# Optimization experiments

Measured on AMD Instinct MI355X. Metric: run time of the kernel, lower is better.

Reference implementation:

```python
import jax, jax.numpy as jnp
import numpy as np

EMBED_DIM = 1024
NUM_HEADS = 16
HEAD_DIM = EMBED_DIM // NUM_HEADS


def setup_inputs() -> dict:
    key = jax.random.key(0)
    ks = jax.random.split(key, 5)
    B, S, D = 2, 2048, EMBED_DIM
    scale = 1.0 / np.sqrt(D)
    x = jax.random.normal(ks[0], (B, S, D), dtype=jnp.float32)
    qkv_w = jax.random.uniform(ks[1], (3 * D, D), dtype=jnp.float32, minval=-scale, maxval=scale)
    qkv_b = jax.random.uniform(ks[2], (3 * D,), dtype=jnp.float32, minval=-scale, maxval=scale)
    out_w = jax.random.uniform(ks[3], (D, D), dtype=jnp.float32, minval=-scale, maxval=scale)
    out_b = jax.random.uniform(ks[4], (D,), dtype=jnp.float32, minval=-scale, maxval=scale)
    return {"x": x, "qkv_w": qkv_w, "qkv_b": qkv_b, "out_w": out_w, "out_b": out_b}


def reference(x, qkv_w, qkv_b, out_w, out_b):
    B, S, D = x.shape
    H, hd = NUM_HEADS, HEAD_DIM
    # QKV projection (torch Linear: y = x @ W^T + b)
    qkv = jnp.einsum('bsd,ed->bse', x, qkv_w) + qkv_b          # [B,S,3D]
    qkv = qkv.reshape(B, S, 3, H, hd)
    q, k, v = (jnp.moveaxis(qkv[:, :, i], 2, 1) for i in range(3))  # each [B,H,S,hd]
    scores = jnp.einsum('bhqd,bhkd->bhqk', q, k) / np.sqrt(hd)  # [B,H,S,S]
    probs = jax.nn.softmax(scores, axis=-1)
    attn = jnp.einsum('bhqk,bhkd->bhqd', probs, v)              # [B,H,S,hd]
    attn = jnp.moveaxis(attn, 1, 2).reshape(B, S, D)
    return jnp.einsum('bsd,ed->bse', attn, out_w) + out_b
```

## Files before the change

### kernel.cpp

```cpp
#include <hip/hip_runtime.h>
#include <stdint.h>

typedef __bf16 bf16;
typedef __attribute__((ext_vector_type(2))) __bf16 bf16x2;
typedef __attribute__((ext_vector_type(4))) __bf16 bf16x4;
typedef __attribute__((ext_vector_type(8))) __bf16 bf16x8;
typedef __attribute__((ext_vector_type(4))) float f32x4;
typedef __attribute__((ext_vector_type(16))) float f32x16;

#define LOG2E_OVER_8 0.18033688011112042f

__device__ __forceinline__ void gl_lds16(const bf16* g, bf16* l) {
  __builtin_amdgcn_global_load_lds(
      (const __attribute__((address_space(1))) void*)g,
      (__attribute__((address_space(3))) void*)l, 16, 0, 0);
}
#define WAIT_VM0_BARRIER() asm volatile("s_waitcnt vmcnt(0)\n\ts_barrier" ::: "memory")

__device__ __forceinline__ uint32_t pack2(float a, float b) {
  union { bf16x2 v; uint32_t u; } z;
  z.v[0] = (bf16)a; z.v[1] = (bf16)b;
  return z.u;
}

__global__ __launch_bounds__(256) void cvt_kernel(const float* __restrict__ s,
                                                  bf16* __restrict__ d, int n) {
  int i = (blockIdx.x * 256 + threadIdx.x) * 8;
  if (i >= n) return;
  float4 a = *(const float4*)(s + i);
  float4 b = *(const float4*)(s + i + 4);
  bf16x8 o;
  o[0] = (bf16)a.x; o[1] = (bf16)a.y; o[2] = (bf16)a.z; o[3] = (bf16)a.w;
  o[4] = (bf16)b.x; o[5] = (bf16)b.y; o[6] = (bf16)b.z; o[7] = (bf16)b.w;
  *(bf16x8*)(d + i) = o;
}

template <int EPI>
__global__ __launch_bounds__(256, 3) void gemm_bt(
    const bf16* __restrict__ A, const bf16* __restrict__ Bw,
    const float* __restrict__ bias,
    bf16* __restrict__ qo, bf16* __restrict__ ko, bf16* __restrict__ vTo,
    float* __restrict__ outF) {
  constexpr int MT = EPI ? 64 : 128;
  constexpr int MI = MT / 32;
  constexpr int ASZ = MT * 32;
  constexpr int BSZ = 128 * 32;
  constexpr int RS = 136;
  constexpr int SME = EPI ? (2 * ASZ + 2 * BSZ) : (128 * RS);
  __shared__ __attribute__((aligned(16))) bf16 smem[SME];

  const int t = threadIdx.x;
  const int L = t & 63;
  const int li = L & 15;
  const int qd = L >> 4;
  const int w = t >> 6;
  const int wm = (w >> 1) * (MT / 2);
  const int wn = (w & 1) * 64;
  const int bm0 = blockIdx.y * MT;
  const int bn0 = blockIdx.x * 128;
  const int r_st = t >> 2;
  const int c_st = (t & 3) * 8;

  const bf16* Ab = A + (size_t)bm0 * 1024;
  const bf16* Bb = Bw + (size_t)bn0 * 1024;

  auto issue = [&](int k0, int bi) {
    bf16* As_ = smem + bi * ASZ;
    bf16* Bs_ = smem + 2 * ASZ + bi * BSZ;
    gl_lds16(Ab + (size_t)r_st * 1024 + k0 + c_st, As_ + t * 8);
    if constexpr (MT == 128)
      gl_lds16(Ab + (size_t)(r_st + 64) * 1024 + k0 + c_st, As_ + (t + 256) * 8);
    gl_lds16(Bb + (size_t)r_st * 1024 + k0 + c_st, Bs_ + t * 8);
    gl_lds16(Bb + (size_t)(r_st + 64) * 1024 + k0 + c_st, Bs_ + (t + 256) * 8);
  };

  f32x4 acc[MI][4] = {};
  issue(0, 0);
  for (int it = 0; it < 32; ++it) {
    WAIT_VM0_BARRIER();
    if (it < 31) issue((it + 1) * 32, (it + 1) & 1);
    const bf16* Ac = smem + (it & 1) * ASZ;
    const bf16* Bc = smem + 2 * ASZ + (it & 1) * BSZ;
    bf16x8 af[MI], bfr[4];
#pragma unroll
    for (int mi = 0; mi < MI; ++mi)
      af[mi] = *(const bf16x8*)(Ac + (wm + mi * 16 + li) * 32 + qd * 8);
#pragma unroll
    for (int ni = 0; ni < 4; ++ni)
      bfr[ni] = *(const bf16x8*)(Bc + (wn + ni * 16 + li) * 32 + qd * 8);
#pragma unroll
    for (int mi = 0; mi < MI; ++mi)
#pragma unroll
      for (int ni = 0; ni < 4; ++ni)
        acc[mi][ni] = __builtin_amdgcn_mfma_f32_16x16x32_bf16(af[mi], bfr[ni],
                                                              acc[mi][ni], 0, 0, 0);
  }

  if constexpr (EPI == 0) {
    const int which = bn0 >> 10;
    __syncthreads();
    bf16* Ct = smem;
    if (which == 2) {
#pragma unroll
      for (int mi = 0; mi < MI; ++mi) {
        const int m_l = wm + mi * 16 + qd * 4;
#pragma unroll
        for (int ni = 0; ni < 4; ++ni) {
          const int n_l = wn + ni * 16 + li;
          const float bi = bias[bn0 + n_l];
          bf16x4 pk;
#pragma unroll
          for (int r = 0; r < 4; ++r) pk[r] = (bf16)(acc[mi][ni][r] + bi);
          *(bf16x4*)(Ct + n_l * RS + m_l) = pk;
        }
      }
    } else {
      const float sc = (which == 0) ? LOG2E_OVER_8 : 1.0f;
#pragma unroll
      for (int mi = 0; mi < MI; ++mi) {
        const int m_l = wm + mi * 16 + qd * 4;
#pragma unroll
        for (int ni = 0; ni < 4; ++ni) {
          const int n_l = wn + ni * 16 + li;
          const float bi = bias[bn0 + n_l];
#pragma unroll
          for (int r = 0; r < 4; ++r)
            Ct[(m_l + r) * RS + n_l] = (bf16)((acc[mi][ni][r] + bi) * sc);
        }
      }
    }
    __syncthreads();
    const int jr = t >> 4;
    const int jc = t & 15;
#pragma unroll
    for (int pass = 0; pass < 8; ++pass) {
      const int row = pass * 16 + jr;
      bf16x8 vv = *(const bf16x8*)(Ct + row * RS + jc * 8);
      if (which == 2) {
        const int n_g = bn0 + row;
        const int hh = (n_g >> 6) & 15, dd = n_g & 63;
        const int bb = bm0 >> 11;
        const int s_b = (bm0 & 2047) + jc * 8;
        *(bf16x8*)(vTo + ((size_t)(bb * 16 + hh) * 64 + dd) * 2048 + s_b) = vv;
      } else {
        const int m_g = bm0 + row;
        const int bb = m_g >> 11, ss = m_g & 2047;
        const int n_g = bn0 + jc * 8;
        const int hh = (n_g >> 6) & 15, dd = n_g & 63;
        bf16* dst = (which == 0 ? qo : ko);
        *(bf16x8*)(dst + ((size_t)(bb * 16 + hh) * 2048 + ss) * 64 + dd) = vv;
      }
    }
  } else {
#pragma unroll
    for (int mi = 0; mi < MI; ++mi) {
      const int m_g = bm0 + wm + mi * 16 + qd * 4;
#pragma unroll
      for (int ni = 0; ni < 4; ++ni) {
        const int n_g = bn0 + wn + ni * 16 + li;
        const float bi = bias[n_g];
#pragma unroll
        for (int r = 0; r < 4; ++r)
          outF[(size_t)(m_g + r) * 1024 + n_g] = acc[mi][ni][r] + bi;
      }
    }
  }
}

__global__ __launch_bounds__(256, 3) void attn_fwd(
    const bf16* __restrict__ Q, const bf16* __restrict__ K,
    const bf16* __restrict__ VT, bf16* __restrict__ AO) {
  __shared__ __attribute__((aligned(16))) bf16 Ks[2 * 4096];
  __shared__ __attribute__((aligned(16))) bf16 Vs[2 * 4096];
  const int t = threadIdx.x;
  const int L = t & 63;
  const int m31 = L & 31;
  const int hi = L >> 5;
  const int w = t >> 6;

  const int lid = blockIdx.x + (blockIdx.y << 4) + (blockIdx.z << 8);
  const int slot = lid >> 3;
  const int bh_ = ((lid & 7) << 2) + (slot >> 4);
  const int qb = slot & 15;
  const int b = bh_ >> 4, h = bh_ & 15;
  const size_t bh = (size_t)(b * 16 + h);

  const bf16* Qp = Q + bh * 2048 * 64;
  const bf16* Kp = K + bh * 2048 * 64;
  const bf16* Vp = VT + bh * 64 * 2048;
  const int q0 = qb * 128 + w * 32;

  bf16x8 qf[4];
#pragma unroll
  for (int s = 0; s < 4; ++s)
    qf[s] = *(const bf16x8*)(Qp + (size_t)(q0 + m31) * 64 + s * 16 + hi * 8);

  f32x16 acc[2] = {};
  float lsum = 0.f;

  const int srow = t >> 3;
  const int scc = (t & 7) ^ (srow & 7);
  auto issue = [&](int kt, int bi) {
    const bf16* Kt = Kp + (size_t)kt * 4096;
    const bf16* Vt = Vp + kt * 64;
    bf16* Kd = Ks + bi * 4096;
    bf16* Vd = Vs + bi * 4096;
    gl_lds16(Kt + srow * 64 + scc * 8, Kd + t * 8);
    gl_lds16(Kt + (srow + 32) * 64 + scc * 8, Kd + (t + 256) * 8);
    gl_lds16(Vt + (size_t)srow * 2048 + scc * 8, Vd + t * 8);
    gl_lds16(Vt + (size_t)(srow + 32) * 2048 + scc * 8, Vd + (t + 256) * 8);
  };

  const int rlow = m31 & 7;
  issue(0, 0);
  for (int kt = 0; kt < 32; ++kt) {
    WAIT_VM0_BARRIER();
    if (kt < 31) issue(kt + 1, (kt + 1) & 1);
    const bf16* Kc = Ks + (kt & 1) * 4096;
    const bf16* Vc = Vs + (kt & 1) * 4096;

    f32x16 st[2];
#pragma unroll
    for (int kt2 = 0; kt2 < 2; ++kt2) {
      f32x16 z = {};
#pragma unroll
      for (int s = 0; s < 4; ++s) {
        bf16x8 kf = *(const bf16x8*)(
            Kc + ((kt2 * 32 + m31) * 8 + ((2 * s + hi) ^ rlow)) * 8);
        z = __builtin_amdgcn_mfma_f32_32x32x16_bf16(kf, qf[s], z, 0, 0, 0);
      }
      st[kt2] = z;
    }

    uint32_t pk[2][8];
#pragma unroll
    for (int kt2 = 0; kt2 < 2; ++kt2)
#pragma unroll
      for (int j = 0; j < 8; ++j) {
        float a = exp2f(st[kt2][2 * j]);
        float c = exp2f(st[kt2][2 * j + 1]);
        lsum += a + c;
        pk[kt2][j] = pack2(a, c);
      }

    uint32_t sw[2][8];
#pragma unroll
    for (int kt2 = 0; kt2 < 2; ++kt2)
#pragma unroll
      for (int j = 0; j < 8; ++j)
        sw[kt2][j] = (uint32_t)__shfl_xor((int)pk[kt2][j], 32);

    union FU { uint32_t u[4]; bf16x8 v; };
    FU af[2][2];
#pragma unroll
    for (int kt2 = 0; kt2 < 2; ++kt2) {
      if (hi == 0) {
        af[kt2][0].u[0] = pk[kt2][0]; af[kt2][0].u[1] = pk[kt2][1];
        af[kt2][0].u[2] = sw[kt2][0]; af[kt2][0].u[3] = sw[kt2][1];
        af[kt2][1].u[0] = pk[kt2][4]; af[kt2][1].u[1] = pk[kt2][5];
        af[kt2][1].u[2] = sw[kt2][4]; af[kt2][1].u[3] = sw[kt2][5];
      } else {
        af[kt2][0].u[0] = sw[kt2][2]; af[kt2][0].u[1] = sw[kt2][3];
        af[kt2][0].u[2] = pk[kt2][2]; af[kt2][0].u[3] = pk[kt2][3];
        af[kt2][1].u[0] = sw[kt2][6]; af[kt2][1].u[1] = sw[kt2][7];
        af[kt2][1].u[2] = pk[kt2][6]; af[kt2][1].u[3] = pk[kt2][7];
      }
    }

#pragma unroll
    for (int dt = 0; dt < 2; ++dt)
#pragma unroll
      for (int kt2 = 0; kt2 < 2; ++kt2)
#pragma unroll
        for (int u = 0; u < 2; ++u) {
          bf16x8 vf = *(const bf16x8*)(
              Vc + ((dt * 32 + m31) * 8 + ((kt2 * 4 + u * 2 + hi) ^ rlow)) * 8);
          acc[dt] = __builtin_amdgcn_mfma_f32_32x32x16_bf16(af[kt2][u].v, vf,
                                                            acc[dt], 0, 0, 0);
        }
  }

  lsum += __shfl_xor(lsum, 32);
  const float inv = 1.f / lsum;

#pragma unroll
  for (int r = 0; r < 16; ++r) {
    const int qrow = (r & 3) + 8 * (r >> 2) + 4 * hi;
    const float invq = __shfl(inv, qrow);
    const size_t base = ((size_t)b * 2048 + q0 + qrow) * 1024 + h * 64 + m31;
    AO[base] = (bf16)(acc[0][r] * invq);
    AO[base + 32] = (bf16)(acc[1][r] * invq);
  }
}

extern "C" void kernel_launch(void* const* d_in, const int* in_sizes, int n_in,
                              void* d_out, int out_size, void* d_ws, size_t ws_size,
                              hipStream_t stream) {
  const float* x = (const float*)d_in[0];
  const float* qkvw = (const float*)d_in[1];
  const float* qkvb = (const float*)d_in[2];
  const float* outw = (const float*)d_in[3];
  const float* outb = (const float*)d_in[4];
  float* out = (float*)d_out;

  bf16* xb = (bf16*)d_ws;
  bf16* wq = xb + (size_t)4096 * 1024;
  bf16* wo = wq + (size_t)3072 * 1024;
  bf16* q = wo + (size_t)1024 * 1024;
  bf16* kk = q + (size_t)2 * 16 * 2048 * 64;
  bf16* vT = kk + (size_t)2 * 16 * 2048 * 64;
  bf16* attn = xb;

  cvt_kernel<<<2048, 256, 0, stream>>>(x, xb, 4096 * 1024);
  cvt_kernel<<<1536, 256, 0, stream>>>(qkvw, wq, 3072 * 1024);
  cvt_kernel<<<512, 256, 0, stream>>>(outw, wo, 1024 * 1024);

  gemm_bt<0><<<dim3(24, 32), 256, 0, stream>>>(xb, wq, qkvb, q, kk, vT, nullptr);
  attn_fwd<<<dim3(16, 16, 2), 256, 0, stream>>>(q, kk, vT, attn);
  gemm_bt<1><<<dim3(8, 64), 256, 0, stream>>>(attn, wo, outb, nullptr, nullptr, nullptr, out);
}
```

Before: 203.3 us.

## Remap GEMM blocks per XCD, halve attention block size, use native exp2

GEMM launches become 1D grids with a block-index remap that groups neighbouring M-tiles onto the same XCD, aiming for better L2 reuse of the shared weight tiles. The attention kernel drops from 256 to 128 threads, each block covering 64 query rows instead of 128, which doubles the block count for more parallelism. Each block now loads its K/V tiles with four loads per thread, so K/V traffic per query row doubles. exp2f is replaced with the hardware exp2 builtin to avoid range-handling code, at the cost of less accurate results for denormal inputs.

```diff
diff --git a/kernel.cpp b/kernel.cpp
--- a/kernel.cpp
+++ b/kernel.cpp
@@ -9,6 +9,12 @@
 typedef __attribute__((ext_vector_type(16))) float f32x16;
 
 #define LOG2E_OVER_8 0.18033688011112042f
+
+#if __has_builtin(__builtin_amdgcn_exp2f)
+#define EXP2(x) __builtin_amdgcn_exp2f(x)
+#else
+#define EXP2(x) exp2f(x)
+#endif
 
 __device__ __forceinline__ void gl_lds16(const bf16* g, bf16* l) {
   __builtin_amdgcn_global_load_lds(
@@ -49,6 +55,14 @@
   constexpr int SME = EPI ? (2 * ASZ + 2 * BSZ) : (128 * RS);
   __shared__ __attribute__((aligned(16))) bf16 smem[SME];
 
+  int bx, by;
+  {
+    const int f = blockIdx.x;
+    const int xcd = f & 7, idx = f >> 3;
+    if constexpr (EPI == 0) { by = xcd * 4 + (idx & 3); bx = idx >> 2; }
+    else                    { by = xcd * 8 + (idx & 7); bx = idx >> 3; }
+  }
+
   const int t = threadIdx.x;
   const int L = t & 63;
   const int li = L & 15;
@@ -56,8 +70,8 @@
   const int w = t >> 6;
   const int wm = (w >> 1) * (MT / 2);
   const int wn = (w & 1) * 64;
-  const int bm0 = blockIdx.y * MT;
-  const int bn0 = blockIdx.x * 128;
+  const int bm0 = by * MT;
+  const int bn0 = bx * 128;
   const int r_st = t >> 2;
   const int c_st = (t & 3) * 8;
 
@@ -167,7 +181,7 @@
   }
 }
 
-__global__ __launch_bounds__(256, 3) void attn_fwd(
+__global__ __launch_bounds__(128, 2) void attn_fwd(
     const bf16* __restrict__ Q, const bf16* __restrict__ K,
     const bf16* __restrict__ VT, bf16* __restrict__ AO) {
   __shared__ __attribute__((aligned(16))) bf16 Ks[2 * 4096];
@@ -178,17 +192,16 @@
   const int hi = L >> 5;
   const int w = t >> 6;
 
-  const int lid = blockIdx.x + (blockIdx.y << 4) + (blockIdx.z << 8);
-  const int slot = lid >> 3;
-  const int bh_ = ((lid & 7) << 2) + (slot >> 4);
-  const int qb = slot & 15;
+  const int lid = blockIdx.x;
+  const int bh_ = ((lid & 7) << 2) + (lid >> 8);
+  const int qb = (lid >> 3) & 31;
   const int b = bh_ >> 4, h = bh_ & 15;
   const size_t bh = (size_t)(b * 16 + h);
 
   const bf16* Qp = Q + bh * 2048 * 64;
   const bf16* Kp = K + bh * 2048 * 64;
   const bf16* Vp = VT + bh * 64 * 2048;
-  const int q0 = qb * 128 + w * 32;
+  const int q0 = qb * 64 + w * 32;
 
   bf16x8 qf[4];
 #pragma unroll
@@ -205,10 +218,11 @@
     const bf16* Vt = Vp + kt * 64;
     bf16* Kd = Ks + bi * 4096;
     bf16* Vd = Vs + bi * 4096;
-    gl_lds16(Kt + srow * 64 + scc * 8, Kd + t * 8);
-    gl_lds16(Kt + (srow + 32) * 64 + scc * 8, Kd + (t + 256) * 8);
-    gl_lds16(Vt + (size_t)srow * 2048 + scc * 8, Vd + t * 8);
-    gl_lds16(Vt + (size_t)(srow + 32) * 2048 + scc * 8, Vd + (t + 256) * 8);
+#pragma unroll
+    for (int r = 0; r < 4; ++r) {
+      gl_lds16(Kt + (srow + 16 * r) * 64 + scc * 8, Kd + (t + 128 * r) * 8);
+      gl_lds16(Vt + (size_t)(srow + 16 * r) * 2048 + scc * 8, Vd + (t + 128 * r) * 8);
+    }
   };
 
   const int rlow = m31 & 7;
@@ -237,8 +251,8 @@
     for (int kt2 = 0; kt2 < 2; ++kt2)
 #pragma unroll
       for (int j = 0; j < 8; ++j) {
-        float a = exp2f(st[kt2][2 * j]);
-        float c = exp2f(st[kt2][2 * j + 1]);
+        float a = EXP2(st[kt2][2 * j]);
+        float c = EXP2(st[kt2][2 * j + 1]);
         lsum += a + c;
         pk[kt2][j] = pack2(a, c);
       }
@@ -315,7 +329,7 @@
   cvt_kernel<<<1536, 256, 0, stream>>>(qkvw, wq, 3072 * 1024);
   cvt_kernel<<<512, 256, 0, stream>>>(outw, wo, 1024 * 1024);
 
-  gemm_bt<0><<<dim3(24, 32), 256, 0, stream>>>(xb, wq, qkvb, q, kk, vT, nullptr);
-  attn_fwd<<<dim3(16, 16, 2), 256, 0, stream>>>(q, kk, vT, attn);
-  gemm_bt<1><<<dim3(8, 64), 256, 0, stream>>>(attn, wo, outb, nullptr, nullptr, nullptr, out);
-}
+  gemm_bt<0><<<768, 256, 0, stream>>>(xb, wq, qkvb, q, kk, vT, nullptr);
+  attn_fwd<<<1024, 128, 0, stream>>>(q, kk, vT, attn);
+  gemm_bt<1><<<512, 256, 0, stream>>>(attn, wo, outb, nullptr, nullptr, nullptr, out);
+}
```

Measured after the change: 192.4 us. -5.4%, faster.
